# Kernel optimization log

Measured on AMD Instinct MI355X. Metric: run time of the kernel, lower is better.

Reference implementation:

```python
import jax, jax.numpy as jnp
import numpy as np

N = 100000
E = 640000
D = 128


def _sage_conv(x, src, dst, Wp, bp, Wl, bl, Wr):
    # project=True: project + relu source features before aggregation
    h = jax.nn.relu(x @ Wp.T + bp)            # [N, D]
    msgs = h[src]                              # [E, D] gather
    summed = jax.ops.segment_sum(msgs, dst, num_segments=N)   # [N, D]
    cnt = jax.ops.segment_sum(jnp.ones((msgs.shape[0],), x.dtype), dst, num_segments=N)
    mean = summed / jnp.maximum(cnt, 1.0)[:, None]
    # lin_l on aggregated neighbors (with bias) + lin_r on root (no bias)
    return mean @ Wl.T + bl + x @ Wr.T


def setup_inputs() -> dict:
    key = jax.random.key(0)
    ks = jax.random.split(key, 16)
    s = 1.0 / np.sqrt(D)
    x = jax.random.normal(ks[0], (N, D), dtype=jnp.float32)
    edge_index = jax.random.randint(ks[1], (2, E), 0, N, dtype=jnp.int64)
    params = {}
    for i, base in enumerate(["conv0", "conv1"]):
        params[base + "_Wp"] = jax.random.uniform(ks[2 + 5 * i], (D, D), jnp.float32, -s, s)
        params[base + "_bp"] = jax.random.uniform(ks[3 + 5 * i], (D,), jnp.float32, -s, s)
        params[base + "_Wl"] = jax.random.uniform(ks[4 + 5 * i], (D, D), jnp.float32, -s, s)
        params[base + "_bl"] = jax.random.uniform(ks[5 + 5 * i], (D,), jnp.float32, -s, s)
        params[base + "_Wr"] = jax.random.uniform(ks[6 + 5 * i], (D, D), jnp.float32, -s, s)
    return {"x": x, "edge_index": edge_index, **params}


def reference(x, edge_index,
              conv0_Wp, conv0_bp, conv0_Wl, conv0_bl, conv0_Wr,
              conv1_Wp, conv1_bp, conv1_Wl, conv1_bl, conv1_Wr):
    src, dst = edge_index[0], edge_index[1]
    h = _sage_conv(x, src, dst, conv0_Wp, conv0_bp, conv0_Wl, conv0_bl, conv0_Wr)
    h = jax.nn.relu(h)
    return _sage_conv(h, src, dst, conv1_Wp, conv1_bp, conv1_Wl, conv1_bl, conv1_Wr)
```

## Files before the change

kernel.cpp:

```cpp
#include <hip/hip_runtime.h>

#define DD 128

typedef _Float16 f16;
typedef __attribute__((ext_vector_type(8))) _Float16 v8h;
typedef __attribute__((ext_vector_type(4))) _Float16 v4h;
typedef __attribute__((ext_vector_type(4))) float f32x4;

static inline int cdiv(int a, int b) { return (a + b - 1) / b; }


__global__ __launch_bounds__(256) void zero_kernel(int* __restrict__ p, int n) {
    int i = blockIdx.x * 256 + threadIdx.x;
    if (i < n) p[i] = 0;
}


__global__ __launch_bounds__(256) void count_kernel(const int* __restrict__ dst, int E,
                                                    int* __restrict__ cnt) {
    int e = blockIdx.x * 256 + threadIdx.x;
    if (e < E) atomicAdd(&cnt[dst[e]], 1);
}

__global__ __launch_bounds__(256) void scan1(const int* __restrict__ cnt, int N,
                                             int* __restrict__ bsum) {
    __shared__ int s[256];
    int i = blockIdx.x * 256 + threadIdx.x;
    s[threadIdx.x] = (i < N) ? cnt[i] : 0;
    __syncthreads();
    for (int off = 128; off > 0; off >>= 1) {
        if (threadIdx.x < off) s[threadIdx.x] += s[threadIdx.x + off];
        __syncthreads();
    }
    if (threadIdx.x == 0) bsum[blockIdx.x] = s[0];
}

__global__ __launch_bounds__(512) void scan2(const int* __restrict__ bsum, int NB,
                                             int* __restrict__ boff) {
    __shared__ int s[512];
    int t = threadIdx.x;
    int v = (t < NB) ? bsum[t] : 0;
    s[t] = v;
    __syncthreads();
    for (int off = 1; off < 512; off <<= 1) {
        int x = (t >= off) ? s[t - off] : 0;
        __syncthreads();
        s[t] += x;
        __syncthreads();
    }
    if (t < NB) boff[t] = s[t] - v;
}

__global__ __launch_bounds__(256) void scan3(const int* __restrict__ cnt,
                                             const int* __restrict__ boff, int N,
                                             int* __restrict__ off) {
    __shared__ int s[256];
    int t = threadIdx.x;
    int i = blockIdx.x * 256 + t;
    int v = (i < N) ? cnt[i] : 0;
    s[t] = v;
    __syncthreads();
    for (int o = 1; o < 256; o <<= 1) {
        int x = (t >= o) ? s[t - o] : 0;
        __syncthreads();
        s[t] += x;
        __syncthreads();
    }
    int excl = s[t] - v + boff[blockIdx.x];
    if (i < N) off[i] = excl;
    if (i == N - 1) off[N] = excl + v;
}

__global__ __launch_bounds__(256) void fill_kernel(const int* __restrict__ src,
                                                   const int* __restrict__ dst, int E,
                                                   const int* __restrict__ off,
                                                   int* __restrict__ cnt,
                                                   int* __restrict__ csr) {
    int e = blockIdx.x * 256 + threadIdx.x;
    if (e < E) {
        int d = dst[e];
        int p = atomicSub(&cnt[d], 1) - 1;
        csr[off[d] + p] = src[e];
    }
}


__global__ __launch_bounds__(256) void cvt_w_kernel(const float* __restrict__ W0,
                                                    const float* __restrict__ W1,
                                                    const float* __restrict__ W2,
                                                    const float* __restrict__ W3,
                                                    const float* __restrict__ W4,
                                                    const float* __restrict__ W5,
                                                    f16* __restrict__ out) {
    int mat = blockIdx.x >> 4;
    const float* W = mat == 0 ? W0 : mat == 1 ? W1 : mat == 2 ? W2
                   : mat == 3 ? W3 : mat == 4 ? W4 : W5;
    int base = (blockIdx.x & 15) * 1024 + threadIdx.x * 4;
    float4 v = *(const float4*)(W + base);
    v4h o;
    o[0] = (f16)v.x; o[1] = (f16)v.y; o[2] = (f16)v.z; o[3] = (f16)v.w;
    *(v4h*)(out + mat * 16384 + base) = o;
}


__global__ __launch_bounds__(256) void aggregate_kernel(const f16* __restrict__ h,
                                                        const int* __restrict__ off,
                                                        const int* __restrict__ csr,
                                                        f16* __restrict__ mean, int N) {
    int n = blockIdx.x * 4 + (threadIdx.x >> 6);
    int l = threadIdx.x & 63;
    int g = l >> 4, c = l & 15;
    if (n >= N) return;
    int s = off[n], e = off[n + 1];
    float acc[8] = {0.f, 0.f, 0.f, 0.f, 0.f, 0.f, 0.f, 0.f};
    int i0 = s + g;
    int i1 = i0 + 4;
    v8h v0 = {}, v1 = {};
    if (i0 < e) v0 = *(const v8h*)(h + (size_t)csr[i0] * DD + c * 8);
    if (i1 < e) v1 = *(const v8h*)(h + (size_t)csr[i1] * DD + c * 8);
    while (i0 < e) {
        int i2 = i1 + 4;
        v8h v2 = {};
        if (i2 < e) v2 = *(const v8h*)(h + (size_t)csr[i2] * DD + c * 8);
#pragma unroll
        for (int j = 0; j < 8; ++j) acc[j] += (float)v0[j];
        v0 = v1;
        v1 = v2;
        i0 = i1;
        i1 = i2;
    }
#pragma unroll
    for (int j = 0; j < 8; ++j) {
        acc[j] += __shfl_xor(acc[j], 16);
        acc[j] += __shfl_xor(acc[j], 32);
    }
    int deg = e - s;
    float inv = 1.0f / (float)(deg > 0 ? deg : 1);
    if (g == 0) {
        v8h o;
#pragma unroll
        for (int j = 0; j < 8; ++j) o[j] = (f16)(acc[j] * inv);
        *(v8h*)(mean + (size_t)n * DD + c * 8) = o;
    }
}


__device__ inline void stage_w(const f16* __restrict__ Wg, f16* __restrict__ smem, int t) {
#pragma unroll
    for (int i = 0; i < 8; ++i) {
        int idx16 = i * 256 + t;
        int col = idx16 >> 4, c16 = idx16 & 15;
        int sc = c16 ^ (col & 7);
        uint4 v = *(const uint4*)(Wg + idx16 * 8);
        *(uint4*)(smem + col * DD + sc * 8) = v;
    }
}

__device__ inline v8h read_b(const f16* __restrict__ smem, int ct, int ki, int l) {
    int col = ct * 16 + (l & 15);
    int c16 = ki * 4 + (l >> 4);
    int sc = c16 ^ (col & 7);
    return *(const v8h*)(smem + col * DD + sc * 8);
}

__device__ inline v8h load_frag16(const f16* __restrict__ A, int row, int kb, int M) {
    if (row >= M) {
        v8h z = {};
        return z;
    }
    return *(const v8h*)(A + (size_t)row * DD + kb);
}


template <typename TA, bool WX>
__global__ __launch_bounds__(256) void proj_gemm(const TA* __restrict__ A,
                                                 const f16* __restrict__ W1,
                                                 const float* __restrict__ bias,
                                                 f16* __restrict__ OUT,
                                                 f16* __restrict__ A16, int M) {
    __shared__ f16 WS[DD * DD];
    int t = threadIdx.x, l = t & 63, w = t >> 6;
    int row0 = blockIdx.x * 128 + w * 32;
    int r = l & 15, cg = l >> 4;

    stage_w(W1, WS, t);

    v8h af[2][4];
#pragma unroll
    for (int rt = 0; rt < 2; ++rt) {
        int row = row0 + rt * 16 + r;
#pragma unroll
        for (int ki = 0; ki < 4; ++ki) {
            int kb = ki * 32 + cg * 8;
            if constexpr (sizeof(TA) == 2) {
                af[rt][ki] = load_frag16(A, row, kb, M);
            } else {
                if (row < M) {
                    float4 a = *(const float4*)(A + (size_t)row * DD + kb);
                    float4 b = *(const float4*)(A + (size_t)row * DD + kb + 4);
                    v8h rr;
                    rr[0] = (f16)a.x; rr[1] = (f16)a.y; rr[2] = (f16)a.z; rr[3] = (f16)a.w;
                    rr[4] = (f16)b.x; rr[5] = (f16)b.y; rr[6] = (f16)b.z; rr[7] = (f16)b.w;
                    af[rt][ki] = rr;
                } else {
                    v8h z = {};
                    af[rt][ki] = z;
                }
            }
            if constexpr (WX) {
                if (row < M) *(v8h*)(A16 + (size_t)row * DD + kb) = af[rt][ki];
            }
        }
    }
    __syncthreads();

    f32x4 acc[2][8];
#pragma unroll
    for (int ct = 0; ct < 8; ++ct) {
        float bv = bias[ct * 16 + r];
        f32x4 b4 = {bv, bv, bv, bv};
        acc[0][ct] = b4;
        acc[1][ct] = b4;
    }

#pragma unroll
    for (int ct = 0; ct < 8; ++ct)
#pragma unroll
        for (int ki = 0; ki < 4; ++ki) {
            v8h b = read_b(WS, ct, ki, l);
            acc[0][ct] = __builtin_amdgcn_mfma_f32_16x16x32_f16(af[0][ki], b, acc[0][ct], 0, 0, 0);
            acc[1][ct] = __builtin_amdgcn_mfma_f32_16x16x32_f16(af[1][ki], b, acc[1][ct], 0, 0, 0);
        }

#pragma unroll
    for (int rt = 0; rt < 2; ++rt)
#pragma unroll
        for (int ct = 0; ct < 8; ++ct)
#pragma unroll
            for (int j = 0; j < 4; ++j) {
                int row = row0 + rt * 16 + cg * 4 + j;
                if (row < M)
                    OUT[(size_t)row * DD + ct * 16 + r] = (f16)fmaxf(acc[rt][ct][j], 0.f);
            }
}


template <typename TO, bool RELU>
__global__ __launch_bounds__(256) void dual_gemm(const f16* __restrict__ A,
                                                 const f16* __restrict__ Wl,
                                                 const float* __restrict__ bias,
                                                 const f16* __restrict__ B,
                                                 const f16* __restrict__ Wr,
                                                 TO* __restrict__ OUT, int M) {
    __shared__ f16 WS[2 * DD * DD];
    int t = threadIdx.x, l = t & 63, w = t >> 6;
    int row0 = blockIdx.x * 128 + w * 32;
    int r = l & 15, cg = l >> 4;

    stage_w(Wl, WS, t);
    stage_w(Wr, WS + DD * DD, t);

    v8h afA[2][4], afB[2][4];
#pragma unroll
    for (int rt = 0; rt < 2; ++rt)
#pragma unroll
        for (int ki = 0; ki < 4; ++ki) {
            int row = row0 + rt * 16 + r, kb = ki * 32 + cg * 8;
            afA[rt][ki] = load_frag16(A, row, kb, M);
            afB[rt][ki] = load_frag16(B, row, kb, M);
        }
    __syncthreads();

    f32x4 acc[2][8];
#pragma unroll
    for (int ct = 0; ct < 8; ++ct) {
        float bv = bias[ct * 16 + r];
        f32x4 b4 = {bv, bv, bv, bv};
        acc[0][ct] = b4;
        acc[1][ct] = b4;
    }

#pragma unroll
    for (int ct = 0; ct < 8; ++ct)
#pragma unroll
        for (int ki = 0; ki < 4; ++ki) {
            v8h b1 = read_b(WS, ct, ki, l);
            acc[0][ct] = __builtin_amdgcn_mfma_f32_16x16x32_f16(afA[0][ki], b1, acc[0][ct], 0, 0, 0);
            acc[1][ct] = __builtin_amdgcn_mfma_f32_16x16x32_f16(afA[1][ki], b1, acc[1][ct], 0, 0, 0);
            v8h b2 = read_b(WS + DD * DD, ct, ki, l);
            acc[0][ct] = __builtin_amdgcn_mfma_f32_16x16x32_f16(afB[0][ki], b2, acc[0][ct], 0, 0, 0);
            acc[1][ct] = __builtin_amdgcn_mfma_f32_16x16x32_f16(afB[1][ki], b2, acc[1][ct], 0, 0, 0);
        }

#pragma unroll
    for (int rt = 0; rt < 2; ++rt)
#pragma unroll
        for (int ct = 0; ct < 8; ++ct)
#pragma unroll
            for (int j = 0; j < 4; ++j) {
                int row = row0 + rt * 16 + cg * 4 + j;
                if (row < M) {
                    float v = acc[rt][ct][j];
                    if (RELU) v = fmaxf(v, 0.f);
                    OUT[(size_t)row * DD + ct * 16 + r] = (TO)v;
                }
            }
}


extern "C" void kernel_launch(void* const* d_in, const int* in_sizes, int n_in,
                              void* d_out, int out_size, void* d_ws, size_t ws_size,
                              hipStream_t stream) {
    const float* x = (const float*)d_in[0];
    const int* ei = (const int*)d_in[1];
    const float* Wp0 = (const float*)d_in[2];
    const float* bp0 = (const float*)d_in[3];
    const float* Wl0 = (const float*)d_in[4];
    const float* bl0 = (const float*)d_in[5];
    const float* Wr0 = (const float*)d_in[6];
    const float* Wp1 = (const float*)d_in[7];
    const float* bp1 = (const float*)d_in[8];
    const float* Wl1 = (const float*)d_in[9];
    const float* bl1 = (const float*)d_in[10];
    const float* Wr1 = (const float*)d_in[11];

    int N = in_sizes[0] / DD;
    int E = in_sizes[1] / 2;
    const int* src = ei;
    const int* dst = ei + E;

    char* ws = (char*)d_ws;
    size_t o = 0;
    auto alloc = [&](size_t bytes) {
        size_t r = o;
        o = (o + bytes + 255) & ~(size_t)255;
        return r;
    };
    f16* w16 = (f16*)(ws + alloc((size_t)6 * DD * DD * 2));
    int* cnt = (int*)(ws + alloc((size_t)N * 4));
    int* off = (int*)(ws + alloc((size_t)(N + 1) * 4));
    int NB = cdiv(N, 256);
    int* bsum = (int*)(ws + alloc((size_t)NB * 4));
    int* boff = (int*)(ws + alloc((size_t)NB * 4));
    int* csr = (int*)(ws + alloc((size_t)E * 4));
    f16* mean = (f16*)(ws + alloc((size_t)N * DD * 2));
    f16* y1 = (f16*)(ws + alloc((size_t)N * DD * 2));
    f16* h = (f16*)d_out;
    f16* x16 = (f16*)((char*)d_out + (size_t)N * DD * 2);
    (void)ws_size;

    zero_kernel<<<NB, 256, 0, stream>>>(cnt, N);
    count_kernel<<<cdiv(E, 256), 256, 0, stream>>>(dst, E, cnt);
    scan1<<<NB, 256, 0, stream>>>(cnt, N, bsum);
    scan2<<<1, 512, 0, stream>>>(bsum, NB, boff);
    scan3<<<NB, 256, 0, stream>>>(cnt, boff, N, off);
    fill_kernel<<<cdiv(E, 256), 256, 0, stream>>>(src, dst, E, off, cnt, csr);

    cvt_w_kernel<<<96, 256, 0, stream>>>(Wp0, Wl0, Wr0, Wp1, Wl1, Wr1, w16);
    const f16* wp0 = w16 + 0 * 16384;
    const f16* wl0 = w16 + 1 * 16384;
    const f16* wr0 = w16 + 2 * 16384;
    const f16* wp1 = w16 + 3 * 16384;
    const f16* wl1 = w16 + 4 * 16384;
    const f16* wr1 = w16 + 5 * 16384;

    int GB = cdiv(N, 128);
    proj_gemm<float, true><<<GB, 256, 0, stream>>>(x, wp0, bp0, h, x16, N);
    aggregate_kernel<<<cdiv(N, 4), 256, 0, stream>>>(h, off, csr, mean, N);
    dual_gemm<f16, true><<<GB, 256, 0, stream>>>(mean, wl0, bl0, x16, wr0, y1, N);
    proj_gemm<f16, false><<<GB, 256, 0, stream>>>(y1, wp1, bp1, h, nullptr, N);
    aggregate_kernel<<<cdiv(N, 4), 256, 0, stream>>>(h, off, csr, mean, N);
    dual_gemm<float, false><<<GB, 256, 0, stream>>>(mean, wl1, bl1, y1, wr1, (float*)d_out, N);
}
```

Measured before the change: 242.6 us.

## Batch aggregation gathers eight-deep and halve dual_gemm shared memory

```diff
diff --git a/kernel.cpp b/kernel.cpp
--- a/kernel.cpp
+++ b/kernel.cpp
@@ -113,21 +113,20 @@
     if (n >= N) return;
     int s = off[n], e = off[n + 1];
     float acc[8] = {0.f, 0.f, 0.f, 0.f, 0.f, 0.f, 0.f, 0.f};
-    int i0 = s + g;
-    int i1 = i0 + 4;
-    v8h v0 = {}, v1 = {};
-    if (i0 < e) v0 = *(const v8h*)(h + (size_t)csr[i0] * DD + c * 8);
-    if (i1 < e) v1 = *(const v8h*)(h + (size_t)csr[i1] * DD + c * 8);
-    while (i0 < e) {
-        int i2 = i1 + 4;
-        v8h v2 = {};
-        if (i2 < e) v2 = *(const v8h*)(h + (size_t)csr[i2] * DD + c * 8);
-#pragma unroll
-        for (int j = 0; j < 8; ++j) acc[j] += (float)v0[j];
-        v0 = v1;
-        v1 = v2;
-        i0 = i1;
-        i1 = i2;
+    for (int base = s; base < e; base += 32) {
+        v8h v[8];
+        float wgt[8];
+#pragma unroll
+        for (int u = 0; u < 8; ++u) {
+            int i = base + g + u * 4;
+            int ic = i < e ? i : (e - 1);
+            wgt[u] = (i < e) ? 1.f : 0.f;
+            v[u] = *(const v8h*)(h + (size_t)csr[ic] * DD + c * 8);
+        }
+#pragma unroll
+        for (int u = 0; u < 8; ++u)
+#pragma unroll
+            for (int j = 0; j < 8; ++j) acc[j] = fmaf(wgt[u], (float)v[u][j], acc[j]);
     }
 #pragma unroll
     for (int j = 0; j < 8; ++j) {
@@ -252,13 +251,12 @@
                                                  const f16* __restrict__ B,
                                                  const f16* __restrict__ Wr,
                                                  TO* __restrict__ OUT, int M) {
-    __shared__ f16 WS[2 * DD * DD];
+    __shared__ f16 WS[DD * DD];
     int t = threadIdx.x, l = t & 63, w = t >> 6;
     int row0 = blockIdx.x * 128 + w * 32;
     int r = l & 15, cg = l >> 4;
 
     stage_w(Wl, WS, t);
-    stage_w(Wr, WS + DD * DD, t);
 
     v8h afA[2][4], afB[2][4];
 #pragma unroll
@@ -284,12 +282,22 @@
     for (int ct = 0; ct < 8; ++ct)
 #pragma unroll
         for (int ki = 0; ki < 4; ++ki) {
-            v8h b1 = read_b(WS, ct, ki, l);
-            acc[0][ct] = __builtin_amdgcn_mfma_f32_16x16x32_f16(afA[0][ki], b1, acc[0][ct], 0, 0, 0);
-            acc[1][ct] = __builtin_amdgcn_mfma_f32_16x16x32_f16(afA[1][ki], b1, acc[1][ct], 0, 0, 0);
-            v8h b2 = read_b(WS + DD * DD, ct, ki, l);
-            acc[0][ct] = __builtin_amdgcn_mfma_f32_16x16x32_f16(afB[0][ki], b2, acc[0][ct], 0, 0, 0);
-            acc[1][ct] = __builtin_amdgcn_mfma_f32_16x16x32_f16(afB[1][ki], b2, acc[1][ct], 0, 0, 0);
+            v8h b = read_b(WS, ct, ki, l);
+            acc[0][ct] = __builtin_amdgcn_mfma_f32_16x16x32_f16(afA[0][ki], b, acc[0][ct], 0, 0, 0);
+            acc[1][ct] = __builtin_amdgcn_mfma_f32_16x16x32_f16(afA[1][ki], b, acc[1][ct], 0, 0, 0);
+        }
+
+    __syncthreads();
+    stage_w(Wr, WS, t);
+    __syncthreads();
+
+#pragma unroll
+    for (int ct = 0; ct < 8; ++ct)
+#pragma unroll
+        for (int ki = 0; ki < 4; ++ki) {
+            v8h b = read_b(WS, ct, ki, l);
+            acc[0][ct] = __builtin_amdgcn_mfma_f32_16x16x32_f16(afB[0][ki], b, acc[0][ct], 0, 0, 0);
+            acc[1][ct] = __builtin_amdgcn_mfma_f32_16x16x32_f16(afB[1][ki], b, acc[1][ct], 0, 0, 0);
         }
 
 #pragma unroll
```

Result: slower. 280.4 us (+15.6%).
